# Kernel tuning notes

Hardware: AMD Instinct MI355X
Metric: run time of the kernel (lower is better)

Reference implementation:

```python
import jax, jax.numpy as jnp
import numpy as np
import math

# batch, seq_len, emb_ch, convlru_hidden_ch, spatial H, W (W must equal H, see diag_embed broadcast)
B, L, E, C, H, W = 4, 32, 64, 96, 32, 32


def setup_inputs():
    key = jax.random.key(0)
    ks = jax.random.split(key, 24)
    r_min, r_max = 0.8, 0.99
    u1 = jax.random.uniform(ks[0], (C, H))
    u2 = jax.random.uniform(ks[1], (C, H))
    nu_log = jnp.log(-0.5 * jnp.log(u1 * (r_max ** 2 - r_min ** 2) + r_min ** 2))
    theta_log = jnp.log(u2 * 2.0 * np.pi)
    lam_abs = jnp.exp(-jnp.exp(nu_log))  # |lambda| = exp(-nu)
    gamma_log = jnp.log(jnp.sqrt(1.0 - lam_abs ** 2))
    params_log = jnp.vstack([nu_log, theta_log, gamma_log]).astype(jnp.float32)

    def w(k, shape, fan_in):
        s = 1.0 / np.sqrt(fan_in)
        return jax.random.uniform(k, shape, minval=-s, maxval=s, dtype=jnp.float32)

    return {
        "x": jax.random.normal(ks[2], (B, L, E, H, W), jnp.float32),
        "mask": jnp.ones((B, L), jnp.float32),
        "params_log": params_log,
        "Wb_r": w(ks[3], (C, E), E), "Wb_i": w(ks[4], (C, E), E),
        "bb_r": w(ks[5], (C,), E), "bb_i": w(ks[6], (C,), E),
        "Wp1_r": w(ks[7], (C, C), C), "Wp1_i": w(ks[8], (C, C), C),
        "bp1_r": w(ks[9], (C,), C), "bp1_i": w(ks[10], (C,), C),
        "Wp2_r": w(ks[11], (C, C), C), "Wp2_i": w(ks[12], (C, C), C),
        "bp2_r": w(ks[13], (C,), C), "bp2_i": w(ks[14], (C,), C),
        "Wc_r": w(ks[15], (E, C), C), "Wc_i": w(ks[16], (E, C), C),
        "bc_r": w(ks[17], (E,), C), "bc_i": w(ks[18], (E,), C),
        "ln_w": jnp.ones((E, H, W), jnp.float32),
        "ln_b": jnp.zeros((E, H, W), jnp.float32),
    }


def _forward(x, mask, params_log, Wb, bb, Wp1, bp1, Wp2, bp2, Wc, bc, ln_w, ln_b):
    nu, theta, gamma = jnp.split(jnp.exp(params_log), 3, axis=0)  # each (C, H)
    lamb = jnp.exp(jnp.complex64(-nu + 1j * theta))               # (C, H)
    xc = x.astype(jnp.complex64)
    # proj_B: 1x1 complex conv == channel einsum
    h = jnp.einsum('blehw,ce->blchw', xc, Wb) + bb[:, None, None]
    h = jnp.fft.fft2(h)  # over last two axes
    h = jnp.einsum('blkhw,ck->blchw', h, Wp1) + bp1[:, None, None]
    eye = jnp.eye(H, dtype=jnp.float32)  # (H, W); requires W == H
    # h * torch.diag_embed(gamma): elementwise mult with a diagonal (C,H,H) matrix
    # -> zeroes off-diagonal spatial entries (faithful to the torch code)
    h = h * (gamma[:, :, None] * eye)
    m = jnp.broadcast_to(mask[:, :, None, None, None], h.shape).astype(jnp.float32)
    log2L = int(math.ceil(math.log2(L)))
    lamb = lamb[None]  # (1, C, H)
    for i in range(1, log2L + 1):
        l = 2 ** i
        if i > 1:
            lamb = jnp.concatenate([lamb, lamb * lamb[-1]], axis=0)  # (l//2, C, H)
        hr = h.reshape(B * L // l, l, C, H, W)
        mr = m.reshape(B * L // l, l, C, H, W)
        h1, h2 = hr[:, : l // 2], hr[:, l // 2:]
        # term[n,j,c,a,b] = lamb[j,c,a] * eye[a,b] * h1[n,-1,c,a,b] * mask[n,l//2-1,c,a,b]
        term = (lamb[None, :, :, :, None] * eye) * h1[:, -1:] * mr[:, l // 2 - 1: l // 2]
        h = jnp.concatenate([h1, h2 + term], axis=1).reshape(B, L, C, H, W)
    h = jnp.fft.ifft2(h)
    h = jnp.einsum('blkhw,ck->blchw', h, Wp2) + bp2[:, None, None]
    h = jnp.einsum('blchw,ec->blehw', h, Wc) + bc[:, None, None]
    h = h.real
    # dropout is identity in eval mode
    mu = jnp.mean(h, axis=(-3, -2, -1), keepdims=True)
    var = jnp.var(h, axis=(-3, -2, -1), keepdims=True)
    h = (h - mu) / jnp.sqrt(var + 1e-5) * ln_w + ln_b
    return h + x


def reference(x, mask, params_log, Wb_r, Wb_i, bb_r, bb_i, Wp1_r, Wp1_i, bp1_r, bp1_i, Wp2_r, Wp2_i, bp2_r, bp2_i, Wc_r, Wc_i, bc_r, bc_i, ln_w, ln_b):
    cx = lambda r, i: (r + 1j * i).astype(jnp.complex64)
    return _forward(x, mask, params_log,
                    cx(Wb_r, Wb_i), cx(bb_r, bb_i),
                    cx(Wp1_r, Wp1_i), cx(bp1_r, bp1_i),
                    cx(Wp2_r, Wp2_i), cx(bp2_r, bp2_i),
                    cx(Wc_r, Wc_i), cx(bc_r, bc_i),
                    ln_w, ln_b)
```

## Files before the change

### kernel.cpp

```cpp
#include <hip/hip_runtime.h>

static constexpr int BL = 128;
static constexpr int OFF_ARE  = 2048;
static constexpr int OFF_AIM  = 8192;
static constexpr int OFF_WRE  = 14336;
static constexpr int OFF_WIM  = 20480;
static constexpr int OFF_LRE  = 26624;
static constexpr int OFF_LIM  = 29696;
static constexpr int OFF_GAM  = 32768;
static constexpr int OFF_BH0R = 35840;
static constexpr int OFF_BH0I = 35936;
static constexpr int OFF_BRR  = 36032;
static constexpr int OFF_QF   = 36096;
static constexpr int OFF_Y    = 560384;

__global__ __launch_bounds__(256) void kA(
    const float* __restrict__ x,
    const float* __restrict__ params_log,
    const float* __restrict__ Wb_r, const float* __restrict__ Wb_i,
    const float* __restrict__ bb_r, const float* __restrict__ bb_i,
    const float* __restrict__ Wp1_r, const float* __restrict__ Wp1_i,
    const float* __restrict__ Wp2_r, const float* __restrict__ Wp2_i,
    const float* __restrict__ Wc_r, const float* __restrict__ Wc_i,
    const float* __restrict__ bp2_r, const float* __restrict__ bp2_i,
    const float* __restrict__ bc_r, float* __restrict__ ws) {
  if (blockIdx.x < 2048) {
    __shared__ float pl[4][1024];
    __shared__ float qsh[4][32];
    __shared__ float ct[32], st[32];
    int wave = threadIdx.x >> 6, lane = threadIdx.x & 63;
    if (threadIdx.x < 32) {
      float sv, cv;
      sincosf((float)threadIdx.x * 0.19634954084936207f, &sv, &cv);
      ct[threadIdx.x] = cv;
      st[threadIdx.x] = sv;
    }
    int plane = blockIdx.x * 4 + wave;
    const float4* xp = (const float4*)(x + (size_t)plane * 1024);
    float4* pl4 = (float4*)pl[wave];
#pragma unroll
    for (int j = 0; j < 4; ++j) pl4[j * 64 + lane] = xp[j * 64 + lane];
    __syncthreads();
    int s = lane & 31, halfw = lane >> 5;
    float acc = 0.f;
#pragma unroll
    for (int u0 = 0; u0 < 16; ++u0) {
      int u = halfw * 16 + u0;
      acc += pl[wave][u * 32 + ((s - u) & 31)];
    }
    acc += __shfl_xor(acc, 32);
    if (lane < 32) qsh[wave][lane] = acc;
    __syncthreads();
    int h = lane & 31;
    const float* T = (lane < 32) ? ct : st;
    float sum = 0.f;
    int m = 0;
#pragma unroll
    for (int s2 = 0; s2 < 32; ++s2) {
      sum += qsh[wave][s2] * T[m];
      m = (m + h) & 31;
    }
    if (lane >= 32) sum = -sum;
    ws[OFF_QF + (size_t)plane * 64 + h * 2 + (lane < 32 ? 0 : 1)] = sum;
  } else {
    int tid = (int)(blockIdx.x - 2048) * 256 + threadIdx.x;
    if (tid < 3072) {
      int i = tid;
      float nu = expf(params_log[i]);
      float th = expf(params_log[3072 + i]);
      float g  = expf(params_log[6144 + i]);
      float rr = expf(-nu);
      ws[OFF_LRE + i] = rr * cosf(th);
      ws[OFF_LIM + i] = rr * sinf(th);
      ws[OFF_GAM + i] = g;
    } else if (tid < 9216) {
      int i = tid - 3072;
      int c = i >> 6, e = i & 63;
      float are = 0.f, aim = 0.f;
      for (int k = 0; k < 96; ++k) {
        float pr = Wp1_r[c * 96 + k], pi = Wp1_i[c * 96 + k];
        float wr = Wb_r[k * 64 + e], wi = Wb_i[k * 64 + e];
        are += pr * wr - pi * wi;
        aim += pr * wi + pi * wr;
      }
      ws[OFF_ARE + i] = are;
      ws[OFF_AIM + i] = aim;
    } else if (tid < 15360) {
      int i = tid - 9216;
      int e = i / 96, c = i - e * 96;
      float are = 0.f, aim = 0.f;
      for (int k = 0; k < 96; ++k) {
        float wr = Wc_r[e * 96 + k], wi = Wc_i[e * 96 + k];
        float pr = Wp2_r[k * 96 + c], pi = Wp2_i[k * 96 + c];
        are += wr * pr - wi * pi;
        aim += wr * pi + wi * pr;
      }
      ws[OFF_WRE + i] = are;
      ws[OFF_WIM + i] = aim;
    } else if (tid < 15456) {
      int c = tid - 15360;
      float re = 0.f, im = 0.f;
      for (int k = 0; k < 96; ++k) {
        float pr = Wp1_r[c * 96 + k], pi = Wp1_i[c * 96 + k];
        float br = bb_r[k], bi = bb_i[k];
        re += pr * br - pi * bi;
        im += pr * bi + pi * br;
      }
      ws[OFF_BH0R + c] = 1024.f * re;
      ws[OFF_BH0I + c] = 1024.f * im;
    } else if (tid < 15520) {
      int e = tid - 15456;
      float re = 0.f;
      for (int k = 0; k < 96; ++k)
        re += Wc_r[e * 96 + k] * bp2_r[k] - Wc_i[e * 96 + k] * bp2_i[k];
      ws[OFF_BRR + e] = re + bc_r[e];
    }
  }
}

__global__ __launch_bounds__(256) void kBC(float* __restrict__ ws,
                                           const float* __restrict__ mask,
                                           const float* __restrict__ bp1_r,
                                           const float* __restrict__ bp1_i) {
  __shared__ float qre[32][65], qim[32][65];
  __shared__ float Yre[48][33], Yim[48][33];
  __shared__ float msh[32];
  int b = blockIdx.x >> 6;
  int h = (blockIdx.x >> 1) & 31;
  int ch = blockIdx.x & 1;
  const float2* qF2 = (const float2*)(ws + OFF_QF);
  for (int i = threadIdx.x; i < 2048; i += 256) {
    int l = i >> 6, e = i & 63;
    float2 v = qF2[(size_t)(b * 2048 + l * 64 + e) * 32 + h];
    qre[l][e] = v.x;
    qim[l][e] = v.y;
  }
  if (threadIdx.x < 32) msh[threadIdx.x] = mask[b * 32 + threadIdx.x];
  __syncthreads();
  int l = threadIdx.x & 31, cg = threadIdx.x >> 5;
  int cbase = ch * 48 + cg * 6;
  float yr[6] = {0.f, 0.f, 0.f, 0.f, 0.f, 0.f};
  float yi[6] = {0.f, 0.f, 0.f, 0.f, 0.f, 0.f};
#pragma unroll 8
  for (int e = 0; e < 64; ++e) {
    float qr = qre[l][e], qi_ = qim[l][e];
#pragma unroll
    for (int k = 0; k < 6; ++k) {
      int c = cbase + k;
      float ar = ws[OFF_ARE + c * 64 + e];
      float ai = ws[OFF_AIM + c * 64 + e];
      yr[k] += ar * qr - ai * qi_;
      yi[k] += ar * qi_ + ai * qr;
    }
  }
#pragma unroll
  for (int k = 0; k < 6; ++k) {
    int c = cbase + k;
    float re = yr[k] + bp1_r[c];
    float im = yi[k] + bp1_i[c];
    if (h == 0) { re += ws[OFF_BH0R + c]; im += ws[OFF_BH0I + c]; }
    float g = ws[OFF_GAM + c * 32 + h];
    Yre[cg * 6 + k][l] = g * re;
    Yim[cg * 6 + k][l] = g * im;
  }
  __syncthreads();
  if (threadIdx.x < 48) {
    int cl = threadIdx.x, c = ch * 48 + cl;
    float lr = ws[OFF_LRE + c * 32 + h], li = ws[OFF_LIM + c * 32 + h];
    float2* Sg = (float2*)(ws + OFF_Y);
    float sr = Yre[cl][0], si = Yim[cl][0];
    Sg[((size_t)(b * 32 + 0) * 96 + c) * 32 + h] = make_float2(sr, si);
    for (int l2 = 1; l2 < 32; ++l2) {
      float mk = msh[l2 - 1];
      float cr = mk * (lr * sr - li * si);
      float ci = mk * (lr * si + li * sr);
      sr = Yre[cl][l2] + cr;
      si = Yim[cl][l2] + ci;
      Sg[((size_t)(b * 32 + l2) * 96 + c) * 32 + h] = make_float2(sr, si);
    }
  }
}

__global__ __launch_bounds__(256) void kDE(const float* __restrict__ x,
                                           const float* __restrict__ lnw,
                                           const float* __restrict__ lnb,
                                           float* __restrict__ ws,
                                           float* __restrict__ out) {
  __shared__ float2 S[96][33];
  __shared__ float2 V[64][33];
  __shared__ float Rsh[64][32];
  __shared__ float ct[32], st[32];
  __shared__ float red[8];
  __shared__ float stats[2];
  int bl = blockIdx.x >> 1, half = blockIdx.x & 1;
  const float2* Sg = (const float2*)(ws + OFF_Y) + (size_t)bl * 3072;
  for (int i = threadIdx.x; i < 3072; i += 256) S[i >> 5][i & 31] = Sg[i];
  if (threadIdx.x < 32) {
    float sv, cv;
    sincosf((float)threadIdx.x * 0.19634954084936207f, &sv, &cv);
    ct[threadIdx.x] = cv;
    st[threadIdx.x] = sv;
  }
  __syncthreads();
  int h = threadIdx.x & 31, g = threadIdx.x >> 5;
  float vr[8] = {0.f, 0.f, 0.f, 0.f, 0.f, 0.f, 0.f, 0.f};
  float vi[8] = {0.f, 0.f, 0.f, 0.f, 0.f, 0.f, 0.f, 0.f};
#pragma unroll 4
  for (int c = 0; c < 96; ++c) {
    float2 s = S[c][h];
#pragma unroll
    for (int k = 0; k < 8; ++k) {
      int e = g + k * 8;
      float wr = ws[OFF_WRE + e * 96 + c];
      float wi = ws[OFF_WIM + e * 96 + c];
      vr[k] += wr * s.x - wi * s.y;
      vi[k] += wr * s.y + wi * s.x;
    }
  }
#pragma unroll
  for (int k = 0; k < 8; ++k) V[g + k * 8][h] = make_float2(vr[k], vi[k]);
  __syncthreads();
  float sum = 0.f, sumsq = 0.f;
  int s2 = threadIdx.x & 31;
#pragma unroll
  for (int k = 0; k < 8; ++k) {
    int el = k * 8 + (threadIdx.x >> 5);
    float acc = 0.f;
    int m = 0;
#pragma unroll
    for (int hh = 0; hh < 32; ++hh) {
      float2 v = V[el][hh];
      acc += v.x * ct[m] - v.y * st[m];
      m = (m + s2) & 31;
    }
    float r = acc * (1.0f / 1024.0f) + ws[OFF_BRR + el];
    Rsh[el][s2] = r;
    sum += r;
    sumsq += r * r;
  }
#pragma unroll
  for (int off = 32; off > 0; off >>= 1) {
    sum += __shfl_down(sum, off);
    sumsq += __shfl_down(sumsq, off);
  }
  int wave = threadIdx.x >> 6, lane = threadIdx.x & 63;
  if (lane == 0) { red[wave] = sum; red[4 + wave] = sumsq; }
  __syncthreads();
  if (threadIdx.x == 0) {
    float s0 = red[0] + red[1] + red[2] + red[3];
    float q0 = red[4] + red[5] + red[6] + red[7];
    float mu = s0 * (1.0f / 2048.0f);
    stats[0] = mu;
    stats[1] = rsqrtf(q0 * (1.0f / 2048.0f) - mu * mu + 1e-5f);
  }
  __syncthreads();
  float mu = stats[0], istd = stats[1];
  const float4* x4 = (const float4*)x;
  const float4* lw4 = (const float4*)lnw;
  const float4* lb4 = (const float4*)lnb;
  float4* o4 = (float4*)out;
  int t = threadIdx.x;
  int u = t >> 3, v0 = (t & 7) * 4;
#pragma unroll 4
  for (int it = 0; it < 32; ++it) {
    int e = half * 32 + it;
    int gid = bl * 16384 + e * 256 + t;
    int rem = e * 256 + t;
    float4 xin = x4[gid];
    float4 lw = lw4[rem];
    float4 lb = lb4[rem];
    float4 o;
    o.x = (Rsh[e][(u + v0) & 31] - mu) * istd * lw.x + lb.x + xin.x;
    o.y = (Rsh[e][(u + v0 + 1) & 31] - mu) * istd * lw.y + lb.y + xin.y;
    o.z = (Rsh[e][(u + v0 + 2) & 31] - mu) * istd * lw.z + lb.z + xin.z;
    o.w = (Rsh[e][(u + v0 + 3) & 31] - mu) * istd * lw.w + lb.w + xin.w;
    o4[gid] = o;
  }
}

extern "C" void kernel_launch(void* const* d_in, const int* in_sizes, int n_in,
                              void* d_out, int out_size, void* d_ws, size_t ws_size,
                              hipStream_t stream) {
  const float* x          = (const float*)d_in[0];
  const float* mask       = (const float*)d_in[1];
  const float* params_log = (const float*)d_in[2];
  const float* Wb_r  = (const float*)d_in[3];
  const float* Wb_i  = (const float*)d_in[4];
  const float* bb_r  = (const float*)d_in[5];
  const float* bb_i  = (const float*)d_in[6];
  const float* Wp1_r = (const float*)d_in[7];
  const float* Wp1_i = (const float*)d_in[8];
  const float* bp1_r = (const float*)d_in[9];
  const float* bp1_i = (const float*)d_in[10];
  const float* Wp2_r = (const float*)d_in[11];
  const float* Wp2_i = (const float*)d_in[12];
  const float* bp2_r = (const float*)d_in[13];
  const float* bp2_i = (const float*)d_in[14];
  const float* Wc_r  = (const float*)d_in[15];
  const float* Wc_i  = (const float*)d_in[16];
  const float* bc_r  = (const float*)d_in[17];
  const float* ln_w  = (const float*)d_in[19];
  const float* ln_b  = (const float*)d_in[20];
  float* ws  = (float*)d_ws;
  float* out = (float*)d_out;

  kA<<<2109, 256, 0, stream>>>(x, params_log, Wb_r, Wb_i, bb_r, bb_i,
                               Wp1_r, Wp1_i, Wp2_r, Wp2_i, Wc_r, Wc_i,
                               bp2_r, bp2_i, bc_r, ws);
  kBC<<<256, 256, 0, stream>>>(ws, mask, bp1_r, bp1_i);
  kDE<<<256, 256, 0, stream>>>(x, ln_w, ln_b, ws, out);
}
```

Baseline: 193.4 us.

## Split projection/layernorm kernel to remove redundant work and widen output stage

The fused projection+layernorm kernel is split into kD, which computes only its half of the output channels and writes partial sums and R to workspace, and kE, which applies layernorm and the residual across 8192 blocks. This removes the duplicated 64-channel projection per block pair and spreads the bandwidth-bound output pass over many more blocks. It adds an extra kernel launch and a global round-trip for R and the statistics.

```diff
diff --git a/kernel.cpp b/kernel.cpp
--- a/kernel.cpp
+++ b/kernel.cpp
@@ -13,6 +13,8 @@
 static constexpr int OFF_BRR  = 36032;
 static constexpr int OFF_QF   = 36096;
 static constexpr int OFF_Y    = 560384;
+static constexpr int OFF_R    = 1871104;
+static constexpr int OFF_ST   = 2133248;
 
 __global__ __launch_bounds__(256) void kA(
     const float* __restrict__ x,
@@ -181,17 +183,11 @@
   }
 }
 
-__global__ __launch_bounds__(256) void kDE(const float* __restrict__ x,
-                                           const float* __restrict__ lnw,
-                                           const float* __restrict__ lnb,
-                                           float* __restrict__ ws,
-                                           float* __restrict__ out) {
-  __shared__ float2 S[96][33];
-  __shared__ float2 V[64][33];
-  __shared__ float Rsh[64][32];
+__global__ __launch_bounds__(256) void kD(float* __restrict__ ws) {
+  __shared__ float2 S[96][32];
+  __shared__ float2 V[32][33];
   __shared__ float ct[32], st[32];
   __shared__ float red[8];
-  __shared__ float stats[2];
   int bl = blockIdx.x >> 1, half = blockIdx.x & 1;
   const float2* Sg = (const float2*)(ws + OFF_Y) + (size_t)bl * 3072;
   for (int i = threadIdx.x; i < 3072; i += 256) S[i >> 5][i & 31] = Sg[i];
@@ -203,14 +199,14 @@
   }
   __syncthreads();
   int h = threadIdx.x & 31, g = threadIdx.x >> 5;
-  float vr[8] = {0.f, 0.f, 0.f, 0.f, 0.f, 0.f, 0.f, 0.f};
-  float vi[8] = {0.f, 0.f, 0.f, 0.f, 0.f, 0.f, 0.f, 0.f};
+  float vr[4] = {0.f, 0.f, 0.f, 0.f}, vi[4] = {0.f, 0.f, 0.f, 0.f};
+  int ebase = half * 32 + g;
 #pragma unroll 4
   for (int c = 0; c < 96; ++c) {
     float2 s = S[c][h];
 #pragma unroll
-    for (int k = 0; k < 8; ++k) {
-      int e = g + k * 8;
+    for (int k = 0; k < 4; ++k) {
+      int e = ebase + k * 8;
       float wr = ws[OFF_WRE + e * 96 + c];
       float wi = ws[OFF_WIM + e * 96 + c];
       vr[k] += wr * s.x - wi * s.y;
@@ -218,13 +214,14 @@
     }
   }
 #pragma unroll
-  for (int k = 0; k < 8; ++k) V[g + k * 8][h] = make_float2(vr[k], vi[k]);
-  __syncthreads();
+  for (int k = 0; k < 4; ++k) V[k * 8 + g][h] = make_float2(vr[k], vi[k]);
+  __syncthreads();
+  float* R = ws + OFF_R + bl * 2048 + half * 1024;
   float sum = 0.f, sumsq = 0.f;
-  int s2 = threadIdx.x & 31;
-#pragma unroll
-  for (int k = 0; k < 8; ++k) {
-    int el = k * 8 + (threadIdx.x >> 5);
+#pragma unroll
+  for (int k = 0; k < 4; ++k) {
+    int idx = k * 256 + threadIdx.x;
+    int el = idx >> 5, s2 = idx & 31;
     float acc = 0.f;
     int m = 0;
 #pragma unroll
@@ -233,8 +230,8 @@
       acc += v.x * ct[m] - v.y * st[m];
       m = (m + s2) & 31;
     }
-    float r = acc * (1.0f / 1024.0f) + ws[OFF_BRR + el];
-    Rsh[el][s2] = r;
+    float r = acc * (1.0f / 1024.0f) + ws[OFF_BRR + half * 32 + el];
+    R[idx] = r;
     sum += r;
     sumsq += r * r;
   }
@@ -247,35 +244,38 @@
   if (lane == 0) { red[wave] = sum; red[4 + wave] = sumsq; }
   __syncthreads();
   if (threadIdx.x == 0) {
-    float s0 = red[0] + red[1] + red[2] + red[3];
-    float q0 = red[4] + red[5] + red[6] + red[7];
-    float mu = s0 * (1.0f / 2048.0f);
-    stats[0] = mu;
-    stats[1] = rsqrtf(q0 * (1.0f / 2048.0f) - mu * mu + 1e-5f);
-  }
-  __syncthreads();
-  float mu = stats[0], istd = stats[1];
-  const float4* x4 = (const float4*)x;
-  const float4* lw4 = (const float4*)lnw;
-  const float4* lb4 = (const float4*)lnb;
-  float4* o4 = (float4*)out;
-  int t = threadIdx.x;
-  int u = t >> 3, v0 = (t & 7) * 4;
-#pragma unroll 4
-  for (int it = 0; it < 32; ++it) {
-    int e = half * 32 + it;
-    int gid = bl * 16384 + e * 256 + t;
-    int rem = e * 256 + t;
-    float4 xin = x4[gid];
-    float4 lw = lw4[rem];
-    float4 lb = lb4[rem];
-    float4 o;
-    o.x = (Rsh[e][(u + v0) & 31] - mu) * istd * lw.x + lb.x + xin.x;
-    o.y = (Rsh[e][(u + v0 + 1) & 31] - mu) * istd * lw.y + lb.y + xin.y;
-    o.z = (Rsh[e][(u + v0 + 2) & 31] - mu) * istd * lw.z + lb.z + xin.z;
-    o.w = (Rsh[e][(u + v0 + 3) & 31] - mu) * istd * lw.w + lb.w + xin.w;
-    o4[gid] = o;
-  }
+    ws[OFF_ST + bl * 4 + half * 2]     = red[0] + red[1] + red[2] + red[3];
+    ws[OFF_ST + bl * 4 + half * 2 + 1] = red[4] + red[5] + red[6] + red[7];
+  }
+}
+
+__global__ __launch_bounds__(256) void kE(const float* __restrict__ x,
+                                          const float* __restrict__ lnw,
+                                          const float* __restrict__ lnb,
+                                          const float* __restrict__ ws,
+                                          float* __restrict__ out) {
+  __shared__ float Rs[32];
+  int bl = blockIdx.x >> 6, e = blockIdx.x & 63;
+  if (threadIdx.x < 32)
+    Rs[threadIdx.x] = ws[OFF_R + bl * 2048 + e * 32 + threadIdx.x];
+  const float* stp = ws + OFF_ST + bl * 4;
+  float s0 = stp[0] + stp[2], q0 = stp[1] + stp[3];
+  float mu = s0 * (1.0f / 2048.0f);
+  float istd = rsqrtf(q0 * (1.0f / 2048.0f) - mu * mu + 1e-5f);
+  __syncthreads();
+  int gid = blockIdx.x * 256 + threadIdx.x;
+  int pos = threadIdx.x * 4;
+  int u = pos >> 5, v = pos & 31;
+  int rem4 = e * 256 + threadIdx.x;
+  const float4 xin = ((const float4*)x)[gid];
+  const float4 lw = ((const float4*)lnw)[rem4];
+  const float4 lb = ((const float4*)lnb)[rem4];
+  float4 o;
+  o.x = (Rs[(u + v) & 31] - mu) * istd * lw.x + lb.x + xin.x;
+  o.y = (Rs[(u + v + 1) & 31] - mu) * istd * lw.y + lb.y + xin.y;
+  o.z = (Rs[(u + v + 2) & 31] - mu) * istd * lw.z + lb.z + xin.z;
+  o.w = (Rs[(u + v + 3) & 31] - mu) * istd * lw.w + lb.w + xin.w;
+  ((float4*)out)[gid] = o;
 }
 
 extern "C" void kernel_launch(void* const* d_in, const int* in_sizes, int n_in,
@@ -308,5 +308,6 @@
                                Wp1_r, Wp1_i, Wp2_r, Wp2_i, Wc_r, Wc_i,
                                bp2_r, bp2_i, bc_r, ws);
   kBC<<<256, 256, 0, stream>>>(ws, mask, bp1_r, bp1_i);
-  kDE<<<256, 256, 0, stream>>>(x, ln_w, ln_b, ws, out);
-}
+  kD<<<256, 256, 0, stream>>>(ws);
+  kE<<<8192, 256, 0, stream>>>(x, ln_w, ln_b, ws, out);
+}
```

New measurement: 178.3 us. 7.8% less time.
